# Kernel tuning notes

Measured on AMD Instinct MI355X. Metric: run time of the kernel, lower is better.

Reference implementation:

```python
import jax, jax.numpy as jnp
import numpy as np

B, H, W, C = 8, 64, 64, 256
EPS = 1e-5


def unfold(img, k, p):
    # img: [B, C, Hh, Ww] -> patches [B, C, k*k, Hh*Ww] (torch.nn.Unfold layout)
    b, c, hh, ww = img.shape
    xp = jnp.pad(img, ((0, 0), (0, 0), (p, p), (p, p)))
    pats = jnp.stack([xp[:, :, i:i + hh, j:j + ww]
                      for i in range(k) for j in range(k)], axis=2)
    return pats.reshape(b, c, k * k, hh * ww)


def fold(cols, k, p, hh, ww):
    # cols: [B, C*k*k, hh*ww] -> scatter-add back to [B, C, hh, ww] (torch.nn.Fold)
    b = cols.shape[0]
    c = cols.shape[1] // (k * k)
    pt = cols.reshape(b, c, k, k, hh, ww)
    out = jnp.zeros((b, c, hh + 2 * p, ww + 2 * p), cols.dtype)
    for i in range(k):
        for j in range(k):
            out = out.at[:, :, i:i + hh, j:j + ww].add(pt[:, :, i, j])
    return out[:, :, p:p + hh, p:p + ww]


def maxpool(img, k, p):
    # same-size max pool, stride 1
    return jax.lax.reduce_window(img, -jnp.inf, jax.lax.max,
                                 (1, 1, k, k), (1, 1, 1, 1),
                                 [(0, 0), (0, 0), (p, p), (p, p)])


def setup_inputs() -> dict:
    key = jax.random.key(0)
    ks = jax.random.split(key, 4)
    x = jax.random.normal(ks[0], (B, H, W, C), dtype=jnp.float32)
    Wv = jax.random.normal(ks[1], (C, C), dtype=jnp.float32) * 0.02
    bv = jnp.zeros((C,), jnp.float32)
    Wa = jax.random.normal(ks[2], (C, 81), dtype=jnp.float32) * 0.02
    ba = jnp.zeros((81,), jnp.float32)
    Wfu = jax.random.normal(ks[3], (2 * C, C), dtype=jnp.float32) * 0.02
    bfu = jnp.zeros((C,), jnp.float32)
    gamma = jnp.ones((C,), jnp.float32)
    beta = jnp.zeros((C,), jnp.float32)
    return {"x": x, "Wv": Wv, "bv": bv, "Wa": Wa, "ba": ba,
            "Wfu": Wfu, "bfu": bfu, "gamma": gamma, "beta": beta}


def reference(x, Wv, bv, Wa, ba, Wfu, bfu, gamma, beta):
    b, h, w, c = x.shape
    x3 = x
    # 3x3 windowed attention branch (5x5 branch in source is dead code: its
    # result is overwritten by `x2 = relu(x)` before use).
    v = x @ Wv + bv                                # [B,H,W,C]
    v_img = jnp.transpose(v, (0, 3, 2, 1))         # [B,C,W,H] (H/W swap as in source)
    pats = unfold(v_img, 3, 1)                     # [B,C,9,W*H]
    v3 = jnp.transpose(pats, (0, 3, 2, 1))         # [B,HW,9,C]
    a = (x @ Wa + ba).reshape(b, h * w, 9, 9)
    a = jax.nn.softmax(a, axis=-1)
    y = jnp.einsum('lbpq,lbqc->lbpc'.replace('l', 'n'), a, v3)  # [B,HW,9,C]
    y = jnp.transpose(y, (0, 3, 2, 1)).reshape(b, c * 9, h * w)
    xf = fold(y, 3, 1, h, w)                       # [B,C,H,W]
    xf = jnp.transpose(xf, (0, 3, 2, 1))           # [B,W,H,C]
    xr = jax.nn.relu(xf)
    x_max = jnp.transpose(x3, (0, 3, 2, 1))        # [B,C,W,H]
    m1 = jnp.transpose(maxpool(x_max, 3, 1), (0, 3, 2, 1))  # [B,H,W,C]
    x1 = jax.nn.relu(xr + m1)
    x2 = jax.nn.relu(x1)
    m2 = jnp.transpose(maxpool(x_max, 5, 2), (0, 3, 2, 1))
    x2 = jax.nn.relu(x2 + m2)
    xfu = jnp.concatenate([x1, x2], axis=-1) @ Wfu + bfu
    xfu = jax.nn.relu(xfu)
    out = x3 + xfu                                 # [B,H,W,C]
    # BatchNorm2d (training mode: batch stats) applied on [B,C,W,H]
    img = jnp.transpose(out, (0, 3, 2, 1))
    mean = img.mean(axis=(0, 2, 3), keepdims=True)
    var = img.var(axis=(0, 2, 3), keepdims=True)
    imgn = (img - mean) * jax.lax.rsqrt(var + EPS)
    imgn = imgn * gamma[None, :, None, None] + beta[None, :, None, None]
    return jnp.transpose(imgn, (0, 2, 3, 1))       # [B,W,H,C]
```

## Files before the change

kernel.cpp:

```cpp
#include <hip/hip_runtime.h>
#include <math.h>

#define NLOC 32768
#define CH 256

typedef __attribute__((ext_vector_type(8))) short short8;
typedef __attribute__((ext_vector_type(4))) float floatx4;

__device__ inline unsigned short f2bf(float x) {
  union { float f; unsigned u; } c; c.f = x;
  unsigned r = c.u + 0x7FFFu + ((c.u >> 16) & 1u);
  return (unsigned short)(r >> 16);
}
__device__ inline float bflo(unsigned u) {
  union { unsigned u; float f; } c; c.u = u << 16; return c.f;
}
__device__ inline float bfhi(unsigned u) {
  union { unsigned u; float f; } c; c.u = u & 0xFFFF0000u; return c.f;
}
__device__ inline float bf2f(unsigned short u) {
  union { unsigned u; float f; } c; c.u = (unsigned)u << 16; return c.f;
}

__device__ __forceinline__ void gl_lds16(const void* g, void* l) {
  __builtin_amdgcn_global_load_lds(
      (const __attribute__((address_space(1))) unsigned int*)g,
      (__attribute__((address_space(3))) unsigned int*)l, 16, 0, 0);
}

__global__ __launch_bounds__(64) void k_pack_w(
    const float* __restrict__ Wv, const float* __restrict__ Wa,
    const float* __restrict__ Wfu, unsigned short* __restrict__ wp) {
  int fid = blockIdx.x;
  int l = threadIdx.x;
  const float* W; int ldn, nvalid, nf, ks;
  if (fid < 128)      { W = Wv;  ldn = 256; nvalid = 256; nf = fid >> 3; ks = fid & 7; }
  else if (fid < 384) { int f = fid - 128; W = Wfu; ldn = 256; nvalid = 256; nf = f >> 4; ks = f & 15; }
  else                { int f = fid - 384; W = Wa;  ldn = 81;  nvalid = 81;  nf = f >> 3; ks = f & 7; }
  unsigned short* dst = wp + (size_t)fid * 512;
  int c = nf * 16 + (l & 15);
  int k0 = ks * 32 + (l >> 4) * 8;
  unsigned short u[8];
#pragma unroll
  for (int j = 0; j < 8; ++j)
    u[j] = (c < nvalid) ? f2bf(W[(size_t)(k0 + j) * ldn + c]) : (unsigned short)0;
  uint4 pk;
  pk.x = u[0] | ((unsigned)u[1] << 16);
  pk.y = u[2] | ((unsigned)u[3] << 16);
  pk.z = u[4] | ((unsigned)u[5] << 16);
  pk.w = u[6] | ((unsigned)u[7] << 16);
  *(uint4*)(dst + l * 8) = pk;
}

__global__ __launch_bounds__(256) void k_pool(
    const float* __restrict__ x, unsigned short* __restrict__ rm3,
    unsigned short* __restrict__ rm5, unsigned short* __restrict__ xb) {
  int tid = threadIdx.x;
  int loc = blockIdx.x * 4 + (tid >> 6);
  int beta = loc & 63;
  int c0 = (tid & 63) * 4;
  const float* base = x + ((size_t)loc - beta) * CH + c0;
  const float NI = -INFINITY;
  float4 r3 = {NI, NI, NI, NI}, r5, xv;
#pragma unroll
  for (int d = -1; d <= 1; ++d) {
    int bb = beta + d;
    if ((unsigned)bb >= 64u) continue;
    float4 f = *(const float4*)(base + (size_t)bb * CH);
    if (d == 0) xv = f;
    r3.x = fmaxf(r3.x, f.x); r3.y = fmaxf(r3.y, f.y);
    r3.z = fmaxf(r3.z, f.z); r3.w = fmaxf(r3.w, f.w);
  }
  r5 = r3;
#pragma unroll
  for (int d = -2; d <= 2; d += 4) {
    int bb = beta + d;
    if ((unsigned)bb >= 64u) continue;
    float4 f = *(const float4*)(base + (size_t)bb * CH);
    r5.x = fmaxf(r5.x, f.x); r5.y = fmaxf(r5.y, f.y);
    r5.z = fmaxf(r5.z, f.z); r5.w = fmaxf(r5.w, f.w);
  }
  size_t o = (size_t)loc * CH + c0;
  uint2 p3, p5, px;
  p3.x = f2bf(r3.x) | ((unsigned)f2bf(r3.y) << 16);
  p3.y = f2bf(r3.z) | ((unsigned)f2bf(r3.w) << 16);
  p5.x = f2bf(r5.x) | ((unsigned)f2bf(r5.y) << 16);
  p5.y = f2bf(r5.z) | ((unsigned)f2bf(r5.w) << 16);
  px.x = f2bf(xv.x) | ((unsigned)f2bf(xv.y) << 16);
  px.y = f2bf(xv.z) | ((unsigned)f2bf(xv.w) << 16);
  *(uint2*)(rm3 + o) = p3;
  *(uint2*)(rm5 + o) = p5;
  *(uint2*)(xb + o) = px;
}

__global__ __launch_bounds__(512) void k_gemm_v(
    const unsigned short* __restrict__ xb, const unsigned short* __restrict__ wvp,
    const float* __restrict__ bv, unsigned short* __restrict__ v) {
  __shared__ unsigned short sA[2][16 * 512];
  __shared__ unsigned short sB[2][16 * 512];
  int tid = threadIdx.x, lane = tid & 63, w = tid >> 6;
  int r0 = (blockIdx.x >> 1) * 128;
  int nc0 = (blockIdx.x & 1) * 128;
  int mh = w >> 1, nq = w & 1;
  floatx4 acc[2][4];
#pragma unroll
  for (int mt = 0; mt < 2; ++mt)
#pragma unroll
    for (int nf = 0; nf < 4; ++nf) acc[mt][nf] = (floatx4)(0.f);
#pragma unroll
  for (int f = 0; f < 4; ++f) {
    int fg = w * 4 + f;
    if (fg < 16) {
      int mt16 = fg >> 1, ks = fg & 1;
      gl_lds16(xb + (size_t)(r0 + mt16 * 16 + (lane & 15)) * CH + ks * 32 + (lane >> 4) * 8,
               &sA[0][fg * 512]);
    } else {
      int g = fg - 16, nf16 = g >> 1, ks = g & 1;
      gl_lds16(wvp + ((size_t)((nc0 >> 4) + nf16) * 8 + ks) * 512 + lane * 8,
               &sB[0][g * 512]);
    }
  }
  __syncthreads();
  for (int kt = 0; kt < 4; ++kt) {
    int cur = kt & 1;
    if (kt < 3) {
      int kn = kt + 1, nb = kn & 1, kkn = kn * 64;
#pragma unroll
      for (int f = 0; f < 4; ++f) {
        int fg = w * 4 + f;
        if (fg < 16) {
          int mt16 = fg >> 1, ks = fg & 1;
          gl_lds16(xb + (size_t)(r0 + mt16 * 16 + (lane & 15)) * CH + kkn + ks * 32 + (lane >> 4) * 8,
                   &sA[nb][fg * 512]);
        } else {
          int g = fg - 16, nf16 = g >> 1, ks = g & 1;
          gl_lds16(wvp + ((size_t)((nc0 >> 4) + nf16) * 8 + kn * 2 + ks) * 512 + lane * 8,
                   &sB[nb][g * 512]);
        }
      }
    }
#pragma unroll
    for (int ks = 0; ks < 2; ++ks) {
      short8 af[2], bf[4];
#pragma unroll
      for (int mt = 0; mt < 2; ++mt)
        af[mt] = *(const short8*)&sA[cur][(((mh * 2 + mt) << 1) + ks) * 512 + lane * 8];
#pragma unroll
      for (int nf = 0; nf < 4; ++nf)
        bf[nf] = *(const short8*)&sB[cur][(((nq * 4 + nf) << 1) + ks) * 512 + lane * 8];
#pragma unroll
      for (int mt = 0; mt < 2; ++mt)
#pragma unroll
        for (int nf = 0; nf < 4; ++nf)
          acc[mt][nf] = __builtin_amdgcn_mfma_f32_16x16x32_bf16(af[mt], bf[nf], acc[mt][nf], 0, 0, 0);
    }
    __syncthreads();
  }
#pragma unroll
  for (int nf = 0; nf < 4; ++nf) {
    int c = nc0 + nq * 64 + nf * 16 + (lane & 15);
    float bb = bv[c];
#pragma unroll
    for (int mt = 0; mt < 2; ++mt) {
      int crow = r0 + mh * 32 + mt * 16 + (lane >> 4) * 4;
#pragma unroll
      for (int i = 0; i < 4; ++i)
        v[(size_t)(crow + i) * CH + c] = f2bf(acc[mt][nf][i] + bb);
    }
  }
}

__global__ __launch_bounds__(256) void k_gemm_a(
    const unsigned short* __restrict__ xb, const unsigned short* __restrict__ wap,
    const float* __restrict__ ba, float* __restrict__ A) {
  __shared__ float lg[64][96];
  int tid = threadIdx.x, lane = tid & 63, w = tid >> 6;
  int mtile = blockIdx.x * 4 + w;
  int r0 = mtile * 16;
  floatx4 acc[6];
#pragma unroll
  for (int i = 0; i < 6; ++i) acc[i] = (floatx4)(0.f);
  const unsigned short* abase = xb + (size_t)(r0 + (lane & 15)) * CH + (lane >> 4) * 8;
  for (int ks = 0; ks < 8; ++ks) {
    short8 af = *(const short8*)(abase + ks * 32);
#pragma unroll
    for (int nf = 0; nf < 6; ++nf) {
      short8 bfr = *(const short8*)(wap + ((size_t)(nf * 8) + ks) * 512 + lane * 8);
      acc[nf] = __builtin_amdgcn_mfma_f32_16x16x32_bf16(af, bfr, acc[nf], 0, 0, 0);
    }
  }
  int lrow = w * 16 + (lane >> 4) * 4;
#pragma unroll
  for (int nf = 0; nf < 6; ++nf) {
    int c = nf * 16 + (lane & 15);
    float bb = (c < 81) ? ba[c] : 0.f;
#pragma unroll
    for (int i = 0; i < 4; ++i)
      lg[lrow + i][c] = acc[nf][i] + bb;
  }
  __syncthreads();
  int loc0 = blockIdx.x * 64;
  for (int it = 0; it < 3; ++it) {
    int idx = tid + it * 256;
    if (idx < 576) {
      int row = idx / 9, g = idx % 9;
      float vals[9];
#pragma unroll
      for (int q = 0; q < 9; ++q) vals[q] = lg[row][g * 9 + q];
      float m = vals[0];
#pragma unroll
      for (int q = 1; q < 9; ++q) m = fmaxf(m, vals[q]);
      float s = 0.f;
#pragma unroll
      for (int q = 0; q < 9; ++q) { vals[q] = __expf(vals[q] - m); s += vals[q]; }
      float inv = 1.f / s;
      float* o = A + (size_t)(loc0 + row) * 81 + g * 9;
#pragma unroll
      for (int q = 0; q < 9; ++q) o[q] = vals[q] * inv;
    }
  }
}

__global__ __launch_bounds__(512) void k_attn(
    const float* __restrict__ A, const unsigned short* __restrict__ v,
    const unsigned short* __restrict__ rm3, const unsigned short* __restrict__ rm5,
    unsigned short* __restrict__ cat) {
  __shared__ unsigned short vs[5 * 12 * CH];
  __shared__ float w5_s[8][25];
  float* a_sf = (float*)vs;
  int tid = threadIdx.x;
  int loc0 = blockIdx.x * 8;
  int b = loc0 >> 12, alpha = (loc0 >> 6) & 63, beta0 = loc0 & 63;
  for (int idx = tid; idx < 8 * 81; idx += 512) {
    int li = idx / 81, t = idx - li * 81;
    int ij = t / 9, i = ij / 3, j = ij % 3;
    int lh = beta0 + li + 1 - i;
    int lw = alpha + 1 - j;
    float val = 0.f;
    if ((unsigned)lh < 64u && (unsigned)lw < 64u)
      val = A[(size_t)(b * 4096 + lh * 64 + lw) * 81 + t];
    a_sf[li * 81 + t] = val;
  }
  __syncthreads();
  if (tid < 200) {
    int li = tid / 25, o = tid - li * 25;
    int dh = o / 5 - 2, dw = o % 5 - 2;
    float s = 0.f;
    int jlo = dh < 0 ? -dh : 0, jhi = dh > 0 ? 2 - dh : 2;
    int ilo = dw < 0 ? -dw : 0, ihi = dw > 0 ? 2 - dw : 2;
    for (int j = jlo; j <= jhi; ++j)
      for (int i = ilo; i <= ihi; ++i)
        s += a_sf[li * 81 + (i * 3 + j) * 9 + ((i + dw) * 3 + (j + dh))];
    w5_s[li][o] = s;
  }
  __syncthreads();
  const unsigned short* vb = v + (size_t)b * 4096 * CH;
  for (int i = tid; i < 1920; i += 512) {
    int row = i / 384, rem = i - row * 384, col = rem >> 5, ch8 = rem & 31;
    int hv = alpha - 2 + row, wv = beta0 - 2 + col;
    uint4 val = {0u, 0u, 0u, 0u};
    if ((unsigned)hv < 64u && (unsigned)wv < 64u)
      val = *(const uint4*)(vb + (size_t)(hv * 64 + wv) * CH + ch8 * 8);
    *(uint4*)(vs + (size_t)(row * 12 + col) * CH + ch8 * 8) = val;
  }
  __syncthreads();
  int li = tid >> 6, tc = tid & 63, c0 = tc * 4;
  int beta = beta0 + li;
  float m1[4], m2[4];
#pragma unroll
  for (int q = 0; q < 4; ++q) { m1[q] = -INFINITY; m2[q] = -INFINITY; }
#pragma unroll
  for (int da = -2; da <= 2; ++da) {
    int aa = alpha + da;
    if ((unsigned)aa >= 64u) continue;
    size_t ro = (size_t)((b * 64 + aa) * 64 + beta) * CH + c0;
    uint2 p5 = *(const uint2*)(rm5 + ro);
    m2[0] = fmaxf(m2[0], bflo(p5.x)); m2[1] = fmaxf(m2[1], bfhi(p5.x));
    m2[2] = fmaxf(m2[2], bflo(p5.y)); m2[3] = fmaxf(m2[3], bfhi(p5.y));
    if (da >= -1 && da <= 1) {
      uint2 p3 = *(const uint2*)(rm3 + ro);
      m1[0] = fmaxf(m1[0], bflo(p3.x)); m1[1] = fmaxf(m1[1], bfhi(p3.x));
      m1[2] = fmaxf(m1[2], bflo(p3.y)); m1[3] = fmaxf(m1[3], bfhi(p3.y));
    }
  }
  float acc[4] = {0.f, 0.f, 0.f, 0.f};
#pragma unroll
  for (int dh = 0; dh < 5; ++dh) {
#pragma unroll
    for (int dw = 0; dw < 5; ++dw) {
      float wgt = w5_s[li][dh * 5 + dw];
      uint2 pk = *(const uint2*)(vs + (size_t)(dh * 12 + li + dw) * CH + c0);
      acc[0] = fmaf(wgt, bflo(pk.x), acc[0]);
      acc[1] = fmaf(wgt, bfhi(pk.x), acc[1]);
      acc[2] = fmaf(wgt, bflo(pk.y), acc[2]);
      acc[3] = fmaf(wgt, bfhi(pk.y), acc[3]);
    }
  }
  unsigned short u1[4], u2[4];
#pragma unroll
  for (int q = 0; q < 4; ++q) {
    float x1v = fmaxf(fmaxf(acc[q], 0.f) + m1[q], 0.f);
    float x2v = fmaxf(x1v + m2[q], 0.f);
    u1[q] = f2bf(x1v);
    u2[q] = f2bf(x2v);
  }
  unsigned short* cp = cat + (size_t)(loc0 + li) * 512 + c0;
  uint2 pk1, pk2;
  pk1.x = u1[0] | ((unsigned)u1[1] << 16); pk1.y = u1[2] | ((unsigned)u1[3] << 16);
  pk2.x = u2[0] | ((unsigned)u2[1] << 16); pk2.y = u2[2] | ((unsigned)u2[3] << 16);
  *(uint2*)(cp) = pk1;
  *(uint2*)(cp + 256) = pk2;
}

__global__ __launch_bounds__(512) void k_fuse(
    const unsigned short* __restrict__ xb, const unsigned short* __restrict__ cat,
    const unsigned short* __restrict__ wfp, const float* __restrict__ bfu,
    unsigned short* __restrict__ outb, float* __restrict__ sums16) {
  __shared__ unsigned short sA[2][16 * 512];
  __shared__ unsigned short sB[2][16 * 512];
  __shared__ float bsum[512];
  int tid = threadIdx.x, lane = tid & 63, w = tid >> 6;
  for (int i = tid; i < 512; i += 512) bsum[i] = 0.f;
  int r0 = (blockIdx.x >> 1) * 128;
  int nc0 = (blockIdx.x & 1) * 128;
  int mh = w >> 1, nq = w & 1;
  floatx4 acc[2][4];
#pragma unroll
  for (int mt = 0; mt < 2; ++mt)
#pragma unroll
    for (int nf = 0; nf < 4; ++nf) acc[mt][nf] = (floatx4)(0.f);
#pragma unroll
  for (int f = 0; f < 4; ++f) {
    int fg = w * 4 + f;
    if (fg < 16) {
      int mt16 = fg >> 1, ks = fg & 1;
      gl_lds16(cat + (size_t)(r0 + mt16 * 16 + (lane & 15)) * 512 + ks * 32 + (lane >> 4) * 8,
               &sA[0][fg * 512]);
    } else {
      int g = fg - 16, nf16 = g >> 1, ks = g & 1;
      gl_lds16(wfp + ((size_t)((nc0 >> 4) + nf16) * 16 + ks) * 512 + lane * 8,
               &sB[0][g * 512]);
    }
  }
  __syncthreads();
  for (int kt = 0; kt < 8; ++kt) {
    int cur = kt & 1;
    if (kt < 7) {
      int kn = kt + 1, nb = kn & 1, kkn = kn * 64;
#pragma unroll
      for (int f = 0; f < 4; ++f) {
        int fg = w * 4 + f;
        if (fg < 16) {
          int mt16 = fg >> 1, ks = fg & 1;
          gl_lds16(cat + (size_t)(r0 + mt16 * 16 + (lane & 15)) * 512 + kkn + ks * 32 + (lane >> 4) * 8,
                   &sA[nb][fg * 512]);
        } else {
          int g = fg - 16, nf16 = g >> 1, ks = g & 1;
          gl_lds16(wfp + ((size_t)((nc0 >> 4) + nf16) * 16 + kn * 2 + ks) * 512 + lane * 8,
                   &sB[nb][g * 512]);
        }
      }
    }
#pragma unroll
    for (int ks = 0; ks < 2; ++ks) {
      short8 af[2], bf[4];
#pragma unroll
      for (int mt = 0; mt < 2; ++mt)
        af[mt] = *(const short8*)&sA[cur][(((mh * 2 + mt) << 1) + ks) * 512 + lane * 8];
#pragma unroll
      for (int nf = 0; nf < 4; ++nf)
        bf[nf] = *(const short8*)&sB[cur][(((nq * 4 + nf) << 1) + ks) * 512 + lane * 8];
#pragma unroll
      for (int mt = 0; mt < 2; ++mt)
#pragma unroll
        for (int nf = 0; nf < 4; ++nf)
          acc[mt][nf] = __builtin_amdgcn_mfma_f32_16x16x32_bf16(af[mt], bf[nf], acc[mt][nf], 0, 0, 0);
    }
    __syncthreads();
  }
#pragma unroll
  for (int nf = 0; nf < 4; ++nf) {
    int c = nc0 + nq * 64 + nf * 16 + (lane & 15);
    float bb = bfu[c];
    float s = 0.f, ss = 0.f;
#pragma unroll
    for (int mt = 0; mt < 2; ++mt) {
      int crow = r0 + mh * 32 + mt * 16 + (lane >> 4) * 4;
#pragma unroll
      for (int i = 0; i < 4; ++i) {
        int r = crow + i;
        float xv = bf2f(xb[(size_t)r * CH + c]);
        float o = xv + fmaxf(acc[mt][nf][i] + bb, 0.f);
        int b_ = r >> 12, al = (r >> 6) & 63, be = r & 63;
        outb[((size_t)(b_ * 64 + be) * 64 + al) * CH + c] = f2bf(o);
        s += o; ss += o * o;
      }
    }
    s += __shfl_xor(s, 16);  s += __shfl_xor(s, 32);
    ss += __shfl_xor(ss, 16); ss += __shfl_xor(ss, 32);
    if (lane < 16) {
      atomicAdd(&bsum[c & 255], s);
      atomicAdd(&bsum[256 + (c & 255)], ss);
    }
  }
  __syncthreads();
  float* bank = sums16 + (size_t)(blockIdx.x & 15) * 512;
  for (int i = tid; i < 512; i += 512) atomicAdd(&bank[i], bsum[i]);
}

__global__ void k_bnprep(const float* __restrict__ sums16,
                         const float* __restrict__ gamma,
                         const float* __restrict__ beta_,
                         float* __restrict__ sc) {
  int c = threadIdx.x;
  float s = 0.f, ss = 0.f;
#pragma unroll
  for (int bk = 0; bk < 16; ++bk) {
    s += sums16[(size_t)bk * 512 + c];
    ss += sums16[(size_t)bk * 512 + 256 + c];
  }
  const float inv_n = 1.f / (float)NLOC;
  float mean = s * inv_n;
  float var = ss * inv_n - mean * mean;
  float scale = gamma[c] * rsqrtf(var + 1e-5f);
  sc[c] = scale;
  sc[256 + c] = beta_[c] - mean * scale;
}

__global__ __launch_bounds__(256) void k_bn(
    const unsigned short* __restrict__ outb, float* __restrict__ outp,
    const float* __restrict__ sc, int n8) {
  __shared__ float s[512];
  const int tid = threadIdx.x;
  for (int i = tid; i < 512; i += 256) s[i] = sc[i];
  __syncthreads();
  for (int i = blockIdx.x * 256 + tid; i < n8; i += gridDim.x * 256) {
    uint4 pk = ((const uint4*)outb)[i];
    int c0 = (i & 31) * 8;
    float4 o0, o1;
    o0.x = bflo(pk.x) * s[c0 + 0] + s[256 + c0 + 0];
    o0.y = bfhi(pk.x) * s[c0 + 1] + s[256 + c0 + 1];
    o0.z = bflo(pk.y) * s[c0 + 2] + s[256 + c0 + 2];
    o0.w = bfhi(pk.y) * s[c0 + 3] + s[256 + c0 + 3];
    o1.x = bflo(pk.z) * s[c0 + 4] + s[256 + c0 + 4];
    o1.y = bfhi(pk.z) * s[c0 + 5] + s[256 + c0 + 5];
    o1.z = bflo(pk.w) * s[c0 + 6] + s[256 + c0 + 6];
    o1.w = bfhi(pk.w) * s[c0 + 7] + s[256 + c0 + 7];
    ((float4*)outp)[i * 2] = o0;
    ((float4*)outp)[i * 2 + 1] = o1;
  }
}

extern "C" void kernel_launch(void* const* d_in, const int* in_sizes, int n_in,
                              void* d_out, int out_size, void* d_ws, size_t ws_size,
                              hipStream_t stream) {
  const float* x     = (const float*)d_in[0];
  const float* Wv    = (const float*)d_in[1];
  const float* bv    = (const float*)d_in[2];
  const float* Wa    = (const float*)d_in[3];
  const float* ba    = (const float*)d_in[4];
  const float* Wfu   = (const float*)d_in[5];
  const float* bfu   = (const float*)d_in[6];
  const float* gamma = (const float*)d_in[7];
  const float* beta_ = (const float*)d_in[8];
  float* out = (float*)d_out;

  float* sums16 = (float*)d_ws;
  float* sc   = sums16 + 16 * 512;
  unsigned short* wp   = (unsigned short*)(sc + 512);
  unsigned short* wvp  = wp;
  unsigned short* wfp  = wp + (size_t)128 * 512;
  unsigned short* wap  = wp + (size_t)384 * 512;
  unsigned short* vbuf = wp + (size_t)432 * 512;
  float* Abuf = (float*)(vbuf + (size_t)NLOC * CH);
  unsigned short* cat = (unsigned short*)(Abuf + (size_t)NLOC * 81);
  unsigned short* rm3 = cat + (size_t)NLOC * 512;
  unsigned short* rm5 = rm3 + (size_t)NLOC * CH;
  unsigned short* xb  = rm5 + (size_t)NLOC * CH;
  unsigned short* outb = vbuf;

  hipMemsetAsync(sums16, 0, 16 * 512 * sizeof(float), stream);

  k_pack_w<<<432, 64, 0, stream>>>(Wv, Wa, Wfu, wp);
  k_pool<<<8192, 256, 0, stream>>>(x, rm3, rm5, xb);
  k_gemm_v<<<512, 512, 0, stream>>>(xb, wvp, bv, vbuf);
  k_gemm_a<<<512, 256, 0, stream>>>(xb, wap, ba, Abuf);
  k_attn<<<4096, 512, 0, stream>>>(Abuf, vbuf, rm3, rm5, cat);
  k_fuse<<<512, 512, 0, stream>>>(xb, cat, wfp, bfu, outb, sums16);
  k_bnprep<<<1, 256, 0, stream>>>(sums16, gamma, beta_, sc);
  k_bn<<<2048, 256, 0, stream>>>(outb, out, sc, NLOC * CH / 8);
}
```

Before: 122.2 us.

## Compute 5x5 attention aggregation with MFMA using banded weight matrix

The k_attn kernel now handles 16 locations per block instead of 8. Its 25-tap weighted sum over the v neighbourhood is recast as a small GEMM: a banded bf16 weight matrix (16 rows x 100 taps, padded to 128) is multiplied against a 5x20 window of v. The v window is staged through direct global-to-LDS loads, with out-of-range taps pointed at a zeroed workspace buffer, and read back with transposed LDS reads into MFMA 16x16x32 instructions. The aim is to replace per-thread scalar FMAs with matrix cores and to halve redundant window loads. The cost is rounding the tap weights to bf16, a larger LDS footprint that limits occupancy, and an extra LDS round trip for the results.

```diff
diff --git a/kernel.cpp b/kernel.cpp
--- a/kernel.cpp
+++ b/kernel.cpp
@@ -224,14 +224,18 @@
 __global__ __launch_bounds__(512) void k_attn(
     const float* __restrict__ A, const unsigned short* __restrict__ v,
     const unsigned short* __restrict__ rm3, const unsigned short* __restrict__ rm5,
-    unsigned short* __restrict__ cat) {
-  __shared__ unsigned short vs[5 * 12 * CH];
-  __shared__ float w5_s[8][25];
-  float* a_sf = (float*)vs;
-  int tid = threadIdx.x;
-  int loc0 = blockIdx.x * 8;
-  int b = loc0 >> 12, alpha = (loc0 >> 6) & 63, beta0 = loc0 & 63;
-  for (int idx = tid; idx < 8 * 81; idx += 512) {
+    const float* __restrict__ zb, unsigned short* __restrict__ cat) {
+  __shared__ unsigned short vs_f[32768];
+  __shared__ float w5_s[16][25];
+  __shared__ unsigned short Wf[2048];
+  float* a_sf = (float*)vs_f;
+  float* sdump = (float*)vs_f;
+  int tid = threadIdx.x, lane = tid & 63, w = tid >> 6;
+  int blk = blockIdx.x;
+  int beta0 = (blk & 3) * 16;
+  int alpha = (blk >> 2) & 63;
+  int b = blk >> 8;
+  for (int idx = tid; idx < 16 * 81; idx += 512) {
     int li = idx / 81, t = idx - li * 81;
     int ij = t / 9, i = ij / 3, j = ij % 3;
     int lh = beta0 + li + 1 - i;
@@ -242,7 +246,7 @@
     a_sf[li * 81 + t] = val;
   }
   __syncthreads();
-  if (tid < 200) {
+  if (tid < 400) {
     int li = tid / 25, o = tid - li * 25;
     int dh = o / 5 - 2, dw = o % 5 - 2;
     float s = 0.f;
@@ -254,62 +258,124 @@
     w5_s[li][o] = s;
   }
   __syncthreads();
+  if (tid < 256) {
+    int ks = tid >> 6, ln = tid & 63;
+    int row = ln & 15, l4 = (ln >> 4) & 3;
+    unsigned short u[8];
+#pragma unroll
+    for (int h = 0; h < 8; ++h) {
+      int sg = ((h >> 2) & 1) * 16 + l4 * 4 + (h & 3);
+      int k = ks * 32 + sg;
+      float val = 0.f;
+      if (k < 100) {
+        int dh = k / 20, t = k - dh * 20;
+        int dwi = t - row;
+        if ((unsigned)dwi < 5u) val = w5_s[row][dh * 5 + dwi];
+      }
+      u[h] = f2bf(val);
+    }
+    uint4 pk;
+    pk.x = u[0] | ((unsigned)u[1] << 16); pk.y = u[2] | ((unsigned)u[3] << 16);
+    pk.z = u[4] | ((unsigned)u[5] << 16); pk.w = u[6] | ((unsigned)u[7] << 16);
+    *(uint4*)(Wf + tid * 8) = pk;
+  }
   const unsigned short* vb = v + (size_t)b * 4096 * CH;
-  for (int i = tid; i < 1920; i += 512) {
-    int row = i / 384, rem = i - row * 384, col = rem >> 5, ch8 = rem & 31;
-    int hv = alpha - 2 + row, wv = beta0 - 2 + col;
-    uint4 val = {0u, 0u, 0u, 0u};
-    if ((unsigned)hv < 64u && (unsigned)wv < 64u)
-      val = *(const uint4*)(vb + (size_t)(hv * 64 + wv) * CH + ch8 * 8);
-    *(uint4*)(vs + (size_t)(row * 12 + col) * CH + ch8 * 8) = val;
-  }
-  __syncthreads();
-  int li = tid >> 6, tc = tid & 63, c0 = tc * 4;
-  int beta = beta0 + li;
-  float m1[4], m2[4];
-#pragma unroll
-  for (int q = 0; q < 4; ++q) { m1[q] = -INFINITY; m2[q] = -INFINITY; }
-#pragma unroll
-  for (int da = -2; da <= 2; ++da) {
-    int aa = alpha + da;
-    if ((unsigned)aa >= 64u) continue;
-    size_t ro = (size_t)((b * 64 + aa) * 64 + beta) * CH + c0;
-    uint2 p5 = *(const uint2*)(rm5 + ro);
-    m2[0] = fmaxf(m2[0], bflo(p5.x)); m2[1] = fmaxf(m2[1], bfhi(p5.x));
-    m2[2] = fmaxf(m2[2], bflo(p5.y)); m2[3] = fmaxf(m2[3], bfhi(p5.y));
-    if (da >= -1 && da <= 1) {
-      uint2 p3 = *(const uint2*)(rm3 + ro);
-      m1[0] = fmaxf(m1[0], bflo(p3.x)); m1[1] = fmaxf(m1[1], bfhi(p3.x));
-      m1[2] = fmaxf(m1[2], bflo(p3.y)); m1[3] = fmaxf(m1[3], bfhi(p3.y));
-    }
-  }
-  float acc[4] = {0.f, 0.f, 0.f, 0.f};
-#pragma unroll
-  for (int dh = 0; dh < 5; ++dh) {
-#pragma unroll
-    for (int dw = 0; dw < 5; ++dw) {
-      float wgt = w5_s[li][dh * 5 + dw];
-      uint2 pk = *(const uint2*)(vs + (size_t)(dh * 12 + li + dw) * CH + c0);
-      acc[0] = fmaf(wgt, bflo(pk.x), acc[0]);
-      acc[1] = fmaf(wgt, bfhi(pk.x), acc[1]);
-      acc[2] = fmaf(wgt, bflo(pk.y), acc[2]);
-      acc[3] = fmaf(wgt, bfhi(pk.y), acc[3]);
-    }
-  }
-  unsigned short u1[4], u2[4];
-#pragma unroll
-  for (int q = 0; q < 4; ++q) {
-    float x1v = fmaxf(fmaxf(acc[q], 0.f) + m1[q], 0.f);
-    float x2v = fmaxf(x1v + m2[q], 0.f);
-    u1[q] = f2bf(x1v);
-    u2[q] = f2bf(x2v);
-  }
-  unsigned short* cp = cat + (size_t)(loc0 + li) * 512 + c0;
-  uint2 pk1, pk2;
-  pk1.x = u1[0] | ((unsigned)u1[1] << 16); pk1.y = u1[2] | ((unsigned)u1[3] << 16);
-  pk2.x = u2[0] | ((unsigned)u2[1] << 16); pk2.y = u2[2] | ((unsigned)u2[3] << 16);
-  *(uint2*)(cp) = pk1;
-  *(uint2*)(cp + 256) = pk2;
+#pragma unroll
+  for (int it = 0; it < 8; ++it) {
+    int m = it * 512 + tid;
+    int q = m & 63, blob = m >> 6;
+    int ksq = blob >> 4, nf = blob & 15;
+    int kp = ((q >> 5) & 1) * 16 + ((q >> 3) & 3) * 4 + ((q >> 1) & 3);
+    int c0 = nf * 16 + (q & 1) * 8;
+    int k = ksq * 32 + kp;
+    const void* src = zb;
+    if (k < 100) {
+      int dh = k / 20, t = k - dh * 20;
+      int hv = alpha - 2 + dh, wv = beta0 - 2 + t;
+      if ((unsigned)hv < 64u && (unsigned)wv < 64u)
+        src = vb + (size_t)(hv * 64 + wv) * CH + c0;
+    }
+    gl_lds16(src, vs_f + (size_t)(it * 512 + w * 64) * 8);
+  }
+  __syncthreads();
+  floatx4 acc[2];
+  acc[0] = (floatx4)(0.f); acc[1] = (floatx4)(0.f);
+  unsigned vsb = (unsigned)(unsigned long long)(const __attribute__((address_space(3))) void*)vs_f;
+#pragma unroll
+  for (int ks = 0; ks < 4; ++ks) {
+    short8 af = *(const short8*)(Wf + ((size_t)ks * 64 + lane) * 8);
+    unsigned long long lo0, hi0, lo1, hi1;
+    unsigned a0 = vsb + (unsigned)((ks * 16 + w * 2) * 1024) + (unsigned)(lane * 8);
+    unsigned a1 = a0 + 1024;
+    asm volatile("ds_read_b64_tr_b16 %0, %2\n\t"
+                 "ds_read_b64_tr_b16 %1, %2 offset:512"
+                 : "=&v"(lo0), "=&v"(hi0) : "v"(a0));
+    asm volatile("ds_read_b64_tr_b16 %0, %2\n\t"
+                 "ds_read_b64_tr_b16 %1, %2 offset:512"
+                 : "=&v"(lo1), "=&v"(hi1) : "v"(a1));
+    asm volatile("s_waitcnt lgkmcnt(0)" ::: "memory");
+    __builtin_amdgcn_sched_barrier(0);
+    union { short8 s; unsigned long long q[2]; } b0, b1;
+    b0.q[0] = lo0; b0.q[1] = hi0;
+    b1.q[0] = lo1; b1.q[1] = hi1;
+    acc[0] = __builtin_amdgcn_mfma_f32_16x16x32_bf16(af, b0.s, acc[0], 0, 0, 0);
+    acc[1] = __builtin_amdgcn_mfma_f32_16x16x32_bf16(af, b1.s, acc[1], 0, 0, 0);
+  }
+  __syncthreads();
+#pragma unroll
+  for (int nfi = 0; nfi < 2; ++nfi) {
+    int ch = w * 32 + nfi * 16 + (lane & 15);
+    int lrow = (lane >> 4) * 4;
+#pragma unroll
+    for (int i = 0; i < 4; ++i)
+      sdump[(lrow + i) * 256 + ch] = acc[nfi][i];
+  }
+  __syncthreads();
+  {
+    int li = tid >> 5, c0 = (tid & 31) * 8;
+    int beta = beta0 + li;
+    float av[8];
+    *(float4*)(av)     = *(const float4*)(sdump + li * 256 + c0);
+    *(float4*)(av + 4) = *(const float4*)(sdump + li * 256 + c0 + 4);
+    float m1[8], m2[8];
+#pragma unroll
+    for (int q = 0; q < 8; ++q) { m1[q] = -INFINITY; m2[q] = -INFINITY; }
+#pragma unroll
+    for (int da = -2; da <= 2; ++da) {
+      int aa = alpha + da;
+      if ((unsigned)aa >= 64u) continue;
+      size_t ro = (size_t)((b * 64 + aa) * 64 + beta) * CH + c0;
+      uint4 p5 = *(const uint4*)(rm5 + ro);
+      m2[0] = fmaxf(m2[0], bflo(p5.x)); m2[1] = fmaxf(m2[1], bfhi(p5.x));
+      m2[2] = fmaxf(m2[2], bflo(p5.y)); m2[3] = fmaxf(m2[3], bfhi(p5.y));
+      m2[4] = fmaxf(m2[4], bflo(p5.z)); m2[5] = fmaxf(m2[5], bfhi(p5.z));
+      m2[6] = fmaxf(m2[6], bflo(p5.w)); m2[7] = fmaxf(m2[7], bfhi(p5.w));
+      if (da >= -1 && da <= 1) {
+        uint4 p3 = *(const uint4*)(rm3 + ro);
+        m1[0] = fmaxf(m1[0], bflo(p3.x)); m1[1] = fmaxf(m1[1], bfhi(p3.x));
+        m1[2] = fmaxf(m1[2], bflo(p3.y)); m1[3] = fmaxf(m1[3], bfhi(p3.y));
+        m1[4] = fmaxf(m1[4], bflo(p3.z)); m1[5] = fmaxf(m1[5], bfhi(p3.z));
+        m1[6] = fmaxf(m1[6], bflo(p3.w)); m1[7] = fmaxf(m1[7], bfhi(p3.w));
+      }
+    }
+    unsigned short u1[8], u2[8];
+#pragma unroll
+    for (int q = 0; q < 8; ++q) {
+      float x1v = fmaxf(fmaxf(av[q], 0.f) + m1[q], 0.f);
+      float x2v = fmaxf(x1v + m2[q], 0.f);
+      u1[q] = f2bf(x1v);
+      u2[q] = f2bf(x2v);
+    }
+    int loc = b * 4096 + alpha * 64 + beta;
+    unsigned short* cp = cat + (size_t)loc * 512 + c0;
+    uint4 pk1, pk2;
+    pk1.x = u1[0] | ((unsigned)u1[1] << 16); pk1.y = u1[2] | ((unsigned)u1[3] << 16);
+    pk1.z = u1[4] | ((unsigned)u1[5] << 16); pk1.w = u1[6] | ((unsigned)u1[7] << 16);
+    pk2.x = u2[0] | ((unsigned)u2[1] << 16); pk2.y = u2[2] | ((unsigned)u2[3] << 16);
+    pk2.z = u2[4] | ((unsigned)u2[5] << 16); pk2.w = u2[6] | ((unsigned)u2[7] << 16);
+    *(uint4*)(cp) = pk1;
+    *(uint4*)(cp + 256) = pk2;
+  }
 }
 
 __global__ __launch_bounds__(512) void k_fuse(
@@ -466,7 +532,8 @@
   float* out = (float*)d_out;
 
   float* sums16 = (float*)d_ws;
-  float* sc   = sums16 + 16 * 512;
+  float* zbf    = sums16 + 16 * 512;
+  float* sc     = zbf + 16;
   unsigned short* wp   = (unsigned short*)(sc + 512);
   unsigned short* wvp  = wp;
   unsigned short* wfp  = wp + (size_t)128 * 512;
@@ -479,13 +546,13 @@
   unsigned short* xb  = rm5 + (size_t)NLOC * CH;
   unsigned short* outb = vbuf;
 
-  hipMemsetAsync(sums16, 0, 16 * 512 * sizeof(float), stream);
+  hipMemsetAsync(sums16, 0, (16 * 512 + 16) * sizeof(float), stream);
 
   k_pack_w<<<432, 64, 0, stream>>>(Wv, Wa, Wfu, wp);
   k_pool<<<8192, 256, 0, stream>>>(x, rm3, rm5, xb);
   k_gemm_v<<<512, 512, 0, stream>>>(xb, wvp, bv, vbuf);
   k_gemm_a<<<512, 256, 0, stream>>>(xb, wap, ba, Abuf);
-  k_attn<<<4096, 512, 0, stream>>>(Abuf, vbuf, rm3, rm5, cat);
+  k_attn<<<2048, 512, 0, stream>>>(Abuf, vbuf, rm3, rm5, zbf, cat);
   k_fuse<<<512, 512, 0, stream>>>(xb, cat, wfp, bfu, outb, sums16);
   k_bnprep<<<1, 256, 0, stream>>>(sums16, gamma, beta_, sc);
   k_bn<<<2048, 256, 0, stream>>>(outb, out, sc, NLOC * CH / 8);
```

New measurement: 126.1 us. 3.2% more time.
